# Performance work log

Hardware: AMD Instinct MI355X
Metric: run time of the kernel (lower is better)

The kernel has to match this reference:

```python
import jax, jax.numpy as jnp
import numpy as np

N, G, HID, LAT, E_RAND = 20000, 3000, 256, 32, 320000
EPS = 1e-8
NEG_SLOPE = 0.2  # PyG GATv2Conv default leaky_relu slope


def _segment_softmax(logits, seg, n):
    # numerically stable softmax over edges grouped by destination node
    m = jax.ops.segment_max(logits, seg, num_segments=n)
    ex = jnp.exp(logits - m[seg])
    s = jax.ops.segment_sum(ex, seg, num_segments=n)
    return ex / (s[seg] + 1e-16)


def _gatv2(x, src, dst, Wl, Wr, att, b, n):
    # GATv2 (heads=1): score = att . leaky_relu(Wl x_j + Wr x_i)
    xl = x @ Wl  # [N, C] source transform (also the message)
    xr = x @ Wr  # [N, C] destination transform
    e = jax.nn.leaky_relu(xl[src] + xr[dst], NEG_SLOPE)  # [E, C]
    logit = e @ att  # [E]
    alpha = _segment_softmax(logit, dst, n)
    out = jax.ops.segment_sum(alpha[:, None] * xl[src], dst, num_segments=n)
    return out + b


def _log_zinb(x, mu, theta, pi):
    theta = theta[None, :]
    softplus_pi = jax.nn.softplus(-pi)
    log_theta_eps = jnp.log(theta + EPS)
    log_theta_mu_eps = jnp.log(theta + mu + EPS)
    pi_theta_log = -pi + theta * (log_theta_eps - log_theta_mu_eps)
    case_zero = jax.nn.softplus(pi_theta_log) - softplus_pi
    case_nz = (-softplus_pi + pi_theta_log
               + x * (jnp.log(mu + EPS) - log_theta_mu_eps)
               + jax.lax.lgamma(x + theta) - jax.lax.lgamma(theta)
               - jax.lax.lgamma(x + 1.0))
    return jnp.where(x < EPS, case_zero, 0.0) + jnp.where(x > EPS, case_nz, 0.0)


def setup_inputs():
    key = jax.random.key(0)
    ks = jax.random.split(key, 14)
    x = jax.random.randint(ks[0], (N, G), 0, 20).astype(jnp.float32)
    er = jax.random.randint(ks[1], (2, E_RAND), 0, N, dtype=jnp.int32)
    loops = jnp.tile(jnp.arange(N, dtype=jnp.int32)[None, :], (2, 1))
    edge_index = jnp.concatenate([er, loops], axis=1)  # [2, 340000] incl self-loops
    noise = jax.random.normal(ks[2], (N, LAT), dtype=jnp.float32)

    def init(k, shape, fan_in):
        return jax.random.normal(k, shape, dtype=jnp.float32) / np.float32(np.sqrt(fan_in))

    Wl1 = init(ks[3], (G, HID), G); Wr1 = init(ks[4], (G, HID), G)
    att1 = init(ks[5], (HID,), HID); b1 = jnp.zeros((HID,), jnp.float32)
    Wl2 = init(ks[6], (HID, 2 * LAT), HID); Wr2 = init(ks[7], (HID, 2 * LAT), HID)
    att2 = init(ks[8], (2 * LAT,), 2 * LAT); b2 = jnp.zeros((2 * LAT,), jnp.float32)
    Wd1 = init(ks[9], (LAT, HID), LAT); bd1 = jnp.zeros((HID,), jnp.float32)
    Wd2 = init(ks[10], (HID, G), HID); bd2 = jnp.zeros((G,), jnp.float32)
    Wdo = init(ks[11], (HID, G), HID); bdo = jnp.zeros((G,), jnp.float32)
    theta = jax.random.uniform(ks[12], (G,), minval=0.5, maxval=2.0, dtype=jnp.float32)
    return dict(x=x, edge_index=edge_index, noise=noise,
                Wl1=Wl1, Wr1=Wr1, att1=att1, b1=b1,
                Wl2=Wl2, Wr2=Wr2, att2=att2, b2=b2,
                Wd1=Wd1, bd1=bd1, Wd2=Wd2, bd2=bd2, Wdo=Wdo, bdo=bdo,
                theta=theta)


def reference(x, edge_index, noise, Wl1, Wr1, att1, b1, Wl2, Wr2, att2, b2,
              Wd1, bd1, Wd2, bd2, Wdo, bdo, theta):
    n = x.shape[0]
    src, dst = edge_index[0], edge_index[1]
    # --- GATv2 encoder ---
    h = _gatv2(x, src, dst, Wl1, Wr1, att1, b1, n)
    h2 = _gatv2(jax.nn.relu(h), src, dst, Wl2, Wr2, att2, b2, n)  # [N, 2*LAT]
    mu_z, logvar = h2[:, :LAT], h2[:, LAT:]
    # --- reparameterize: std = sqrt(exp(logvar)) ---
    z = mu_z + noise * jnp.exp(0.5 * logvar)
    # --- ZINB decoder ---
    hd = z @ Wd1 + bd1
    mean = jax.nn.softplus(hd @ Wd2 + bd2)
    pi = hd @ Wdo + bdo
    # --- loss: -E[log ZINB] + KL(q(z|x) || N(0,I)) ---
    recon = -jnp.mean(jnp.sum(_log_zinb(x, mean, theta, pi), axis=1))
    kl = jnp.mean(0.5 * jnp.sum(mu_z ** 2 + jnp.exp(logvar) - logvar - 1.0, axis=1))
    return recon + kl
```

## Files before the change

kernel.cpp:

```cpp
#include <hip/hip_runtime.h>
#include <math.h>

#define NN   20000
#define GG   3000
#define HIDD 256
#define LATT 32
#define FEPS 1e-8f

typedef __attribute__((ext_vector_type(8))) __bf16 bf16x8;
typedef __attribute__((ext_vector_type(4))) float f32x4;

__device__ __forceinline__ float fsp(float v) {
    float t = __expf(-fabsf(v));
    return fmaxf(v, 0.f) + __logf(1.f + t);
}
__device__ __forceinline__ float sp_approx(float t) {
    float a = fabsf(t);
    float den = fmaf(a, fmaf(a, fmaf(a, 0.8382f, -1.4958f), 1.87f), 1.f);
    return fmaxf(t, 0.f) + 0.6931472f * __builtin_amdgcn_rcpf(den);
}
__device__ __forceinline__ float lrelu(float v) {
    return v > 0.f ? v : 0.2f * v;
}
__device__ __forceinline__ ushort f2bf(float f) {
    uint b = __float_as_uint(f);
    return (ushort)((b + 0x7FFFu + ((b >> 16) & 1u)) >> 16);
}
__device__ __forceinline__ uint pk2(float a, float b) {
    return (uint)f2bf(a) | ((uint)f2bf(b) << 16);
}
__device__ __forceinline__ void gload16(const void* g, void* l) {
    __builtin_amdgcn_global_load_lds((const __attribute__((address_space(1))) void*)g,
                                     (__attribute__((address_space(3))) void*)l, 16, 0, 0);
}

__global__ void zinb_table(const float* __restrict__ theta, float* __restrict__ tabL,
                           float* __restrict__ logte, int G_) {
    int idx = blockIdx.x * blockDim.x + threadIdx.x;
    if (idx >= G_ * 20) return;
    int g = idx / 20, c = idx % 20;
    float th = theta[g];
    tabL[idx] = lgammaf((float)c + th) - lgammaf(th) - lgammaf((float)c + 1.f);
    if (c == 0) logte[g] = logf(th + FEPS);
}

__global__ void edge_hist(const int* __restrict__ ei, int* __restrict__ cnt, int E) {
    int e = blockIdx.x * blockDim.x + threadIdx.x;
    if (e < E) atomicAdd(&cnt[ei[E + e]], 1);
}

__global__ __launch_bounds__(1024)
void scan_deg(int* __restrict__ cnt_cur, int* __restrict__ rowptr, int Nn) {
    __shared__ int ts[1024];
    int t = threadIdx.x;
    int chunk = (Nn + 1023) / 1024;
    int beg = t * chunk, end = min(beg + chunk, Nn);
    int s = 0;
    for (int i = beg; i < end; i++) s += cnt_cur[i];
    ts[t] = s;
    __syncthreads();
    for (int off = 1; off < 1024; off <<= 1) {
        int v = (t >= off) ? ts[t - off] : 0;
        __syncthreads();
        ts[t] += v;
        __syncthreads();
    }
    int run = (t == 0) ? 0 : ts[t - 1];
    for (int i = beg; i < end; i++) {
        int c = cnt_cur[i];
        rowptr[i] = run;
        cnt_cur[i] = run;
        run += c;
    }
    if (t == 1023) rowptr[Nn] = ts[1023];
}

__global__ void edge_scatter(const int* __restrict__ ei, int* __restrict__ cur,
                             int* __restrict__ eidx, int E) {
    int e = blockIdx.x * blockDim.x + threadIdx.x;
    if (e < E) {
        int p = atomicAdd(&cur[ei[E + e]], 1);
        eidx[p] = e;
    }
}

__global__ __launch_bounds__(256)
void transp_bf16(const float* __restrict__ in, ushort* __restrict__ out,
                 int K, int N, int Kpad) {
    __shared__ ushort t[32][33];
    int k0 = blockIdx.x * 32, n0 = blockIdx.y * 32;
    int tx = threadIdx.x & 31, ty = threadIdx.x >> 5;
    #pragma unroll
    for (int u = 0; u < 32; u += 8) {
        int k = k0 + ty + u, n = n0 + tx;
        t[ty + u][tx] = (k < K && n < N) ? f2bf(in[(size_t)k * N + n]) : (ushort)0;
    }
    __syncthreads();
    #pragma unroll
    for (int u = 0; u < 32; u += 8) {
        int n = n0 + ty + u, k = k0 + tx;
        if (n < N && k < Kpad) out[(size_t)n * Kpad + k] = t[tx][ty + u];
    }
}

template<bool ABF, bool ZEP>
__global__ __launch_bounds__(512, 4)
void gemm_big(const void* __restrict__ Ap, const ushort* __restrict__ B1t,
              const ushort* __restrict__ B2t, float* __restrict__ C1,
              float* __restrict__ C2, const float* __restrict__ xg,
              const float* __restrict__ tabL, const float* __restrict__ theta,
              const float* __restrict__ logte, const float* __restrict__ bd2,
              const float* __restrict__ bdo, double* __restrict__ partsR,
              int M, int Kreal, int Kpad, int Nc) {
    __shared__ __align__(16) char lds[49152];
    char* ldsA  = lds;
    char* ldsB1 = lds + 16384;
    char* ldsB2 = lds + 32768;
    __shared__ float tabs[ZEP ? 128 * 20 : 1];
    __shared__ float thetas[ZEP ? 128 : 1], thltes[ZEP ? 128 : 1];
    __shared__ float bd2s[ZEP ? 128 : 1], bdos[ZEP ? 128 : 1];
    __shared__ double redd[8];

    const int tid = threadIdx.x;
    const int nwg = gridDim.x * gridDim.y;
    const int orig = blockIdx.y * gridDim.x + blockIdx.x;
    const int q = nwg >> 3, r = nwg & 7, xcd = orig & 7;
    const int vv = (xcd < r ? xcd * (q + 1) : r * (q + 1) + (xcd - r) * q) + (orig >> 3);
    const int bx = vv % gridDim.x, by = vv / gridDim.x;
    const int m0 = by * 128, n0 = bx * 128;
    const int lane = tid & 63, wid = tid >> 6;
    const int wr = wid >> 2, wc = wid & 3;
    const int frow = lane & 15;
    const int fkb = (lane >> 4) << 4;

    if (ZEP) {
        for (int i = tid; i < 128; i += 512) {
            int g = n0 + i;
            bool ok = g < Nc;
            float th = ok ? theta[g] : 1.f;
            thetas[i] = th;
            thltes[i] = ok ? th * logte[g] : 0.f;
            bd2s[i]   = ok ? bd2[g] : 0.f;
            bdos[i]   = ok ? bdo[g] : 0.f;
        }
        for (int i = tid; i < 128 * 20; i += 512) {
            int g = n0 + i / 20;
            tabs[i] = (g < Nc) ? tabL[(size_t)g * 20 + i % 20] : 0.f;
        }
    }

    f32x4 acc1[4][2], acc2[4][2];
    #pragma unroll
    for (int i = 0; i < 4; i++)
        #pragma unroll
        for (int j = 0; j < 2; j++) {
            acc1[i][j] = (f32x4){0.f, 0.f, 0.f, 0.f};
            acc2[i][j] = (f32x4){0.f, 0.f, 0.f, 0.f};
        }

    const int row_in = lane >> 3;
    const int sch = (lane & 7) ^ (row_in & 7);
    const int ldso = (lane << 4);

    const int nk = Kpad >> 6;
    for (int t = 0; t < nk; t++) {
        const int k0 = t << 6;
        #pragma unroll
        for (int u = 0; u < 2; u++) {
            int s = (wid << 1) + u;
            int grow = n0 + (s << 3) + row_in;
            if (grow > Nc - 1) grow = Nc - 1;
            size_t go = (size_t)grow * Kpad + k0 + (sch << 3);
            gload16(B1t + go, ldsB1 + (s << 10) + ldso);
            gload16(B2t + go, ldsB2 + (s << 10) + ldso);
        }
        if (ABF) {
            #pragma unroll
            for (int u = 0; u < 2; u++) {
                int s = (wid << 1) + u;
                int grow = m0 + (s << 3) + row_in;
                if (grow > M - 1) grow = M - 1;
                size_t go = (size_t)grow * Kpad + k0 + (sch << 3);
                gload16((const ushort*)Ap + go, ldsA + (s << 10) + ldso);
            }
        } else {
            int arow = tid >> 2;
            int acol = (tid & 3) << 4;
            int gm = m0 + arow;
            uint4 w0 = make_uint4(0u, 0u, 0u, 0u), w1 = w0;
            if (gm < M) {
                const float* af = (const float*)Ap + (size_t)gm * Kreal + k0 + acol;
                if (k0 + 64 <= Kreal) {
                    float4 a = ((const float4*)af)[0];
                    float4 b = ((const float4*)af)[1];
                    float4 c = ((const float4*)af)[2];
                    float4 d = ((const float4*)af)[3];
                    w0.x = pk2(a.x, a.y); w0.y = pk2(a.z, a.w);
                    w0.z = pk2(b.x, b.y); w0.w = pk2(b.z, b.w);
                    w1.x = pk2(c.x, c.y); w1.y = pk2(c.z, c.w);
                    w1.z = pk2(d.x, d.y); w1.w = pk2(d.z, d.w);
                } else {
                    float tmp[16];
                    #pragma unroll
                    for (int jj = 0; jj < 16; jj++) {
                        int gk = k0 + acol + jj;
                        tmp[jj] = (gk < Kreal) ? af[jj] : 0.f;
                    }
                    w0.x = pk2(tmp[0], tmp[1]);  w0.y = pk2(tmp[2], tmp[3]);
                    w0.z = pk2(tmp[4], tmp[5]);  w0.w = pk2(tmp[6], tmp[7]);
                    w1.x = pk2(tmp[8], tmp[9]);  w1.y = pk2(tmp[10], tmp[11]);
                    w1.z = pk2(tmp[12], tmp[13]); w1.w = pk2(tmp[14], tmp[15]);
                }
            }
            int o0 = ((arow << 7) + (acol << 1)) ^ ((arow & 7) << 4);
            int o1 = ((arow << 7) + ((acol + 8) << 1)) ^ ((arow & 7) << 4);
            *(uint4*)(ldsA + o0) = w0;
            *(uint4*)(ldsA + o1) = w1;
        }
        __syncthreads();
        #pragma unroll
        for (int kk = 0; kk < 2; kk++) {
            int kb = (kk << 6) + fkb;
            bf16x8 af[4], b1f[2], b2f[2];
            #pragma unroll
            for (int mi = 0; mi < 4; mi++) {
                int rr = (wr << 6) + (mi << 4) + frow;
                int o = ((rr << 7) + kb) ^ ((rr & 7) << 4);
                af[mi] = *(const bf16x8*)(ldsA + o);
            }
            #pragma unroll
            for (int ni = 0; ni < 2; ni++) {
                int rr = (wc << 5) + (ni << 4) + frow;
                int o = ((rr << 7) + kb) ^ ((rr & 7) << 4);
                b1f[ni] = *(const bf16x8*)(ldsB1 + o);
                b2f[ni] = *(const bf16x8*)(ldsB2 + o);
            }
            #pragma unroll
            for (int mi = 0; mi < 4; mi++)
                #pragma unroll
                for (int ni = 0; ni < 2; ni++) {
                    acc1[mi][ni] = __builtin_amdgcn_mfma_f32_16x16x32_bf16(af[mi], b1f[ni], acc1[mi][ni], 0, 0, 0);
                    acc2[mi][ni] = __builtin_amdgcn_mfma_f32_16x16x32_bf16(af[mi], b2f[ni], acc2[mi][ni], 0, 0, 0);
                }
        }
        __syncthreads();
    }

    const int lr = (lane >> 4) << 2;
    if (!ZEP) {
        #pragma unroll
        for (int mi = 0; mi < 4; mi++)
            #pragma unroll
            for (int ni = 0; ni < 2; ni++) {
                int gmb = m0 + (wr << 6) + (mi << 4) + lr;
                int gn  = n0 + (wc << 5) + (ni << 4) + frow;
                if (gn >= Nc) continue;
                f32x4 v1 = acc1[mi][ni], v2 = acc2[mi][ni];
                #pragma unroll
                for (int j = 0; j < 4; j++) {
                    int gm = gmb + j;
                    if (gm < M) {
                        C1[(size_t)gm * Nc + gn] = v1[j];
                        C2[(size_t)gm * Nc + gn] = v2[j];
                    }
                }
            }
    } else {
        float lsum = 0.f;
        #pragma unroll
        for (int mi = 0; mi < 4; mi++)
            #pragma unroll
            for (int ni = 0; ni < 2; ni++) {
                int lcol = (wc << 5) + (ni << 4) + frow;
                int gn = n0 + lcol;
                int lrow0 = (wr << 6) + (mi << 4) + lr;
                if (gn >= Nc) continue;
                f32x4 am = acc1[mi][ni], ap = acc2[mi][ni];
                float th = thetas[lcol], thlte = thltes[lcol];
                float bm = bd2s[lcol], bp = bdos[lcol];
                #pragma unroll
                for (int j = 0; j < 4; j++) {
                    int gm = m0 + lrow0 + j;
                    if (gm >= M) continue;
                    float mu  = fsp(am[j] + bm);
                    float pi  = ap[j] + bp;
                    float spp = fsp(pi);
                    float ltme = __logf(th + mu + FEPS);
                    float lmu  = __logf(mu + FEPS);
                    float xv = xg[(size_t)gm * Nc + gn];
                    int xi = (int)(xv + 0.5f);
                    float ptl = fmaf(-th, ltme, thlte) - pi;
                    float corr = (xv < FEPS) ? sp_approx(-ptl) : 0.f;
                    lsum += thlte + tabs[lcol * 20 + xi] - spp
                          - (th + xv) * ltme + xv * lmu + corr;
                }
            }
        #pragma unroll
        for (int off = 32; off; off >>= 1) lsum += __shfl_down(lsum, off);
        if (lane == 0) redd[wid] = (double)lsum;
        __syncthreads();
        if (tid == 0) {
            double s = 0.0;
            #pragma unroll
            for (int i = 0; i < 8; i++) s += redd[i];
            partsR[by * gridDim.x + bx] = s;
        }
    }
}

template<bool ABF, bool ZEP>
__global__ __launch_bounds__(256, 4)
void mfma_dual(const void* __restrict__ Ap, const ushort* __restrict__ B1t,
               const ushort* __restrict__ B2t, float* __restrict__ C1,
               float* __restrict__ C2, int M, int K, int Nc) {
    __shared__ __align__(16) char lds[24576];
    char* ldsA  = lds;
    char* ldsB1 = lds + 8192;
    char* ldsB2 = lds + 16384;

    const int tid = threadIdx.x;
    const int m0 = blockIdx.y * 64, n0 = blockIdx.x * 64;
    const int lane = tid & 63, wid = tid >> 6;
    const int wr = wid >> 1, wc = wid & 1;
    const int frow = lane & 15;
    const int fkb = (lane >> 4) << 4;

    f32x4 acc1[2][2], acc2[2][2];
    #pragma unroll
    for (int i = 0; i < 2; i++)
        #pragma unroll
        for (int j = 0; j < 2; j++) {
            acc1[i][j] = (f32x4){0.f, 0.f, 0.f, 0.f};
            acc2[i][j] = (f32x4){0.f, 0.f, 0.f, 0.f};
        }

    const int nk = (K + 63) >> 6;
    for (int t = 0; t < nk; t++) {
        const int k0 = t << 6;
        #pragma unroll
        for (int u = 0; u < 2; u++) {
            int c = tid + (u << 8);
            int row = c >> 3, col8 = (c & 7) << 3;
            int gm = m0 + row, gk = k0 + col8;
            uint4 w = make_uint4(0u, 0u, 0u, 0u);
            if (gm < M && gk < K)
                w = *(const uint4*)((const ushort*)Ap + (size_t)gm * K + gk);
            int o = ((row << 7) + (col8 << 1)) ^ ((row & 7) << 4);
            *(uint4*)(ldsA + o) = w;
        }
        #pragma unroll
        for (int u = 0; u < 2; u++) {
            int c = tid + (u << 8);
            int row = c >> 3, col8 = (c & 7) << 3;
            int gn = n0 + row, gk = k0 + col8;
            uint4 w1 = make_uint4(0u, 0u, 0u, 0u), w2 = w1;
            if (gn < Nc && gk < K) {
                size_t o = (size_t)gn * K + gk;
                w1 = *(const uint4*)(B1t + o);
                w2 = *(const uint4*)(B2t + o);
            }
            int o = ((row << 7) + (col8 << 1)) ^ ((row & 7) << 4);
            *(uint4*)(ldsB1 + o) = w1;
            *(uint4*)(ldsB2 + o) = w2;
        }
        __syncthreads();
        #pragma unroll
        for (int kk = 0; kk < 2; kk++) {
            int kb = (kk << 6) + fkb;
            bf16x8 af[2], b1f[2], b2f[2];
            #pragma unroll
            for (int mi = 0; mi < 2; mi++) {
                int rr = (wr << 5) + (mi << 4) + frow;
                int o = ((rr << 7) + kb) ^ ((rr & 7) << 4);
                af[mi] = *(const bf16x8*)(ldsA + o);
            }
            #pragma unroll
            for (int ni = 0; ni < 2; ni++) {
                int rr = (wc << 5) + (ni << 4) + frow;
                int o = ((rr << 7) + kb) ^ ((rr & 7) << 4);
                b1f[ni] = *(const bf16x8*)(ldsB1 + o);
                b2f[ni] = *(const bf16x8*)(ldsB2 + o);
            }
            #pragma unroll
            for (int mi = 0; mi < 2; mi++)
                #pragma unroll
                for (int ni = 0; ni < 2; ni++) {
                    acc1[mi][ni] = __builtin_amdgcn_mfma_f32_16x16x32_bf16(af[mi], b1f[ni], acc1[mi][ni], 0, 0, 0);
                    acc2[mi][ni] = __builtin_amdgcn_mfma_f32_16x16x32_bf16(af[mi], b2f[ni], acc2[mi][ni], 0, 0, 0);
                }
        }
        __syncthreads();
    }

    const int lr = (lane >> 4) << 2;
    #pragma unroll
    for (int mi = 0; mi < 2; mi++)
        #pragma unroll
        for (int ni = 0; ni < 2; ni++) {
            int gmb = m0 + (wr << 5) + (mi << 4) + lr;
            int gn  = n0 + (wc << 5) + (ni << 4) + frow;
            if (gn >= Nc) continue;
            f32x4 v1 = acc1[mi][ni], v2 = acc2[mi][ni];
            #pragma unroll
            for (int j = 0; j < 4; j++) {
                int gm = gmb + j;
                if (gm < M) {
                    C1[(size_t)gm * Nc + gn] = v1[j];
                    C2[(size_t)gm * Nc + gn] = v2[j];
                }
            }
        }
}

template<int DW, int OM>
__global__ __launch_bounds__(256)
void gat_attn(const float* __restrict__ xl, const float* __restrict__ xr,
              const float* __restrict__ att, const int* __restrict__ ei,
              const int* __restrict__ rowptr, const int* __restrict__ eidx,
              const float* __restrict__ bias, void* __restrict__ out,
              int D, int Nn) {
    __shared__ float lbuf[4][64];
    int wid = threadIdx.x >> 6, lane = threadIdx.x & 63;
    int n = blockIdx.x * 4 + wid;
    if (n >= Nn) return;
    int k = lane * DW;
    float xrr[DW], ats[DW], hacc[DW];
    if (DW == 4) {
        float4 a4 = *(const float4*)(att + k);
        float4 r4 = *(const float4*)(xr + (size_t)n * D + k);
        ats[0] = a4.x; ats[1] = a4.y; ats[2] = a4.z; ats[3] = a4.w;
        xrr[0] = r4.x; xrr[1] = r4.y; xrr[2] = r4.z; xrr[3] = r4.w;
    } else {
        ats[0] = att[k];
        xrr[0] = xr[(size_t)n * D + k];
    }
    #pragma unroll
    for (int d = 0; d < DW; d++) hacc[d] = 0.f;
    float m = -3.0e38f, ssum = 0.f;
    int beg = rowptr[n], end = rowptr[n + 1];
    for (int c0 = beg; c0 < end; c0 += 64) {
        int cnt = min(64, end - c0);
        for (int j = 0; j < cnt; j++) {
            int e = eidx[c0 + j];
            const float* xs = xl + (size_t)ei[e] * D + k;
            float p;
            if (DW == 4) {
                float4 v = *(const float4*)xs;
                p = ats[0] * lrelu(v.x + xrr[0]) + ats[1] * lrelu(v.y + xrr[1])
                  + ats[2] * lrelu(v.z + xrr[2]) + ats[3] * lrelu(v.w + xrr[3]);
            } else {
                p = ats[0] * lrelu(xs[0] + xrr[0]);
            }
            #pragma unroll
            for (int o2 = 32; o2; o2 >>= 1) p += __shfl_down(p, o2);
            if (lane == 0) lbuf[wid][j] = p;
        }
        float cm = (lane < cnt) ? lbuf[wid][lane] : -3.0e38f;
        #pragma unroll
        for (int o2 = 32; o2; o2 >>= 1) cm = fmaxf(cm, __shfl_xor(cm, o2));
        float mnew = fmaxf(m, cm);
        float scale = __expf(m - mnew);
        ssum *= scale;
        #pragma unroll
        for (int d = 0; d < DW; d++) hacc[d] *= scale;
        for (int j = 0; j < cnt; j++) {
            int e = eidx[c0 + j];
            float w = __expf(lbuf[wid][j] - mnew);
            ssum += w;
            const float* xs = xl + (size_t)ei[e] * D + k;
            if (DW == 4) {
                float4 v = *(const float4*)xs;
                hacc[0] = fmaf(w, v.x, hacc[0]);
                hacc[1] = fmaf(w, v.y, hacc[1]);
                hacc[2] = fmaf(w, v.z, hacc[2]);
                hacc[3] = fmaf(w, v.w, hacc[3]);
            } else {
                hacc[0] = fmaf(w, xs[0], hacc[0]);
            }
        }
        m = mnew;
    }
    float inv = 1.f / (ssum + 1e-16f);
    if (DW == 4) {
        float4 b = *(const float4*)(bias + k);
        float r0 = fmaf(hacc[0], inv, b.x), r1 = fmaf(hacc[1], inv, b.y);
        float r2 = fmaf(hacc[2], inv, b.z), r3 = fmaf(hacc[3], inv, b.w);
        if (OM == 0) {
            *(float4*)((float*)out + (size_t)n * D + k) = make_float4(r0, r1, r2, r3);
        } else {
            ushort4 o;
            o.x = f2bf(fmaxf(r0, 0.f)); o.y = f2bf(fmaxf(r1, 0.f));
            o.z = f2bf(fmaxf(r2, 0.f)); o.w = f2bf(fmaxf(r3, 0.f));
            *(ushort4*)((ushort*)out + (size_t)n * D + k) = o;
        }
    } else {
        float r0 = fmaf(hacc[0], inv, bias[k]);
        if (OM == 0) ((float*)out)[(size_t)n * D + k] = r0;
        else         ((ushort*)out)[(size_t)n * D + k] = f2bf(fmaxf(r0, 0.f));
    }
}

__global__ __launch_bounds__(256)
void z_kl(const float* __restrict__ h2, const float* __restrict__ noise,
          float* __restrict__ z, double* __restrict__ partsK, int Nn) {
    __shared__ double rd[4];
    int gid = blockIdx.x * blockDim.x + threadIdx.x;
    int n = gid >> 5, k = gid & 31;
    float kt = 0.f;
    if (n < Nn) {
        float mu = h2[(size_t)n * 64 + k];
        float lv = h2[(size_t)n * 64 + 32 + k];
        float ev = expf(lv);
        z[(size_t)n * 32 + k] = mu + noise[(size_t)n * 32 + k] * expf(0.5f * lv);
        kt = 0.5f * (mu * mu + ev - lv - 1.f);
    }
    #pragma unroll
    for (int off = 32; off; off >>= 1) kt += __shfl_down(kt, off);
    int wid = threadIdx.x >> 6, lane = threadIdx.x & 63;
    if (lane == 0) rd[wid] = (double)kt;
    __syncthreads();
    if (threadIdx.x == 0) partsK[blockIdx.x] = rd[0] + rd[1] + rd[2] + rd[3];
}

__global__ __launch_bounds__(256)
void hd_gemm(const float* __restrict__ z, const float* __restrict__ Wd1,
             const float* __restrict__ bd1, ushort* __restrict__ hd, int Nn) {
    __shared__ float Ws[32 * 256];
    __shared__ float zs[32 * 32];
    int tid = threadIdx.x;
    #pragma unroll
    for (int i = 0; i < 32; i++) Ws[i * 256 + tid] = Wd1[i * 256 + tid];
    int r0 = blockIdx.x * 32;
    for (int i = tid; i < 32 * 32; i += 256) {
        int r = i >> 5, c = i & 31;
        zs[i] = (r0 + r < Nn) ? z[(size_t)(r0 + r) * 32 + c] : 0.f;
    }
    __syncthreads();
    float b = bd1[tid];
    for (int r = 0; r < 32; r++) {
        if (r0 + r >= Nn) break;
        float acc = b;
        #pragma unroll
        for (int k2 = 0; k2 < 32; k2++) acc = fmaf(zs[r * 32 + k2], Ws[k2 * 256 + tid], acc);
        hd[(size_t)(r0 + r) * 256 + tid] = f2bf(acc);
    }
}

__global__ __launch_bounds__(256)
void final_reduce(const double* __restrict__ pR, int nR,
                  const double* __restrict__ pK, int nK,
                  float* __restrict__ out, int Nn) {
    __shared__ double sd[256];
    double s = 0.0;
    for (int i = threadIdx.x; i < nR; i += 256) s -= pR[i];
    for (int i = threadIdx.x; i < nK; i += 256) s += pK[i];
    sd[threadIdx.x] = s;
    __syncthreads();
    for (int o = 128; o; o >>= 1) {
        if (threadIdx.x < o) sd[threadIdx.x] += sd[threadIdx.x + o];
        __syncthreads();
    }
    if (threadIdx.x == 0) out[0] = (float)(sd[0] / (double)Nn);
}

extern "C" void kernel_launch(void* const* d_in, const int* in_sizes, int n_in,
                              void* d_out, int out_size, void* d_ws, size_t ws_size,
                              hipStream_t stream) {
    const int N_ = NN, G_ = GG, HID_ = HIDD;
    const int KP1 = 3008;
    const float* x     = (const float*)d_in[0];
    const int*   ei    = (const int*)d_in[1];
    const float* noise = (const float*)d_in[2];
    const float* Wl1   = (const float*)d_in[3];
    const float* Wr1   = (const float*)d_in[4];
    const float* att1  = (const float*)d_in[5];
    const float* b1    = (const float*)d_in[6];
    const float* Wl2   = (const float*)d_in[7];
    const float* Wr2   = (const float*)d_in[8];
    const float* att2  = (const float*)d_in[9];
    const float* b2    = (const float*)d_in[10];
    const float* Wd1   = (const float*)d_in[11];
    const float* bd1   = (const float*)d_in[12];
    const float* Wd2   = (const float*)d_in[13];
    const float* bd2   = (const float*)d_in[14];
    const float* Wdo   = (const float*)d_in[15];
    const float* bdo   = (const float*)d_in[16];
    const float* theta = (const float*)d_in[17];
    const int E = in_sizes[1] / 2;

    const int MB128 = (N_ + 127) / 128;
    const int DGX   = (G_ + 127) / 128;
    const int nR    = DGX * MB128;
    const int nKb   = (N_ * 32) / 256;

    char* base = (char*)d_ws;
    size_t off = 0;
    auto alloc = [&](size_t bytes) -> char* {
        char* p = base + off;
        off = (off + bytes + 255) & ~(size_t)255;
        return p;
    };
    double* partsR = (double*)alloc((size_t)nR * 8);
    double* partsK = (double*)alloc((size_t)nKb * 8);
    float*  tabL  = (float*)alloc((size_t)G_ * 20 * 4);
    float*  logte = (float*)alloc((size_t)G_ * 4);
    int*    rowptr= (int*)alloc((size_t)(N_ + 1) * 4);
    int*    cur   = (int*)alloc((size_t)N_ * 4);
    int*    eidx  = (int*)alloc((size_t)E * 4);
    ushort* Wl1t  = (ushort*)alloc((size_t)HID_ * KP1 * 2);
    ushort* Wr1t  = (ushort*)alloc((size_t)HID_ * KP1 * 2);
    ushort* Wl2t  = (ushort*)alloc((size_t)64 * HID_ * 2);
    ushort* Wr2t  = (ushort*)alloc((size_t)64 * HID_ * 2);
    ushort* Wd2t  = (ushort*)alloc((size_t)G_ * HID_ * 2);
    ushort* Wdot  = (ushort*)alloc((size_t)G_ * HID_ * 2);
    float*  xl1   = (float*)alloc((size_t)N_ * HID_ * 4);
    float*  xr1   = (float*)alloc((size_t)N_ * HID_ * 4);
    ushort* h_bf  = (ushort*)alloc((size_t)N_ * HID_ * 2);
    float*  xl2   = (float*)alloc((size_t)N_ * 64 * 4);
    float*  xr2   = (float*)alloc((size_t)N_ * 64 * 4);
    float*  h2    = (float*)alloc((size_t)N_ * 64 * 4);
    float*  zb    = (float*)alloc((size_t)N_ * 32 * 4);

    ushort* hdb = (ushort*)xr1;
    float*  outf = (float*)d_out;

    hipMemsetAsync(cur, 0, N_ * sizeof(int), stream);

    zinb_table<<<(G_ * 20 + 255) / 256, 256, 0, stream>>>(theta, tabL, logte, G_);
    edge_hist<<<(E + 255) / 256, 256, 0, stream>>>(ei, cur, E);
    scan_deg<<<1, 1024, 0, stream>>>(cur, rowptr, N_);
    edge_scatter<<<(E + 255) / 256, 256, 0, stream>>>(ei, cur, eidx, E);

    transp_bf16<<<dim3(KP1 / 32, (HID_ + 31) / 32), 256, 0, stream>>>(Wl1, Wl1t, G_, HID_, KP1);
    transp_bf16<<<dim3(KP1 / 32, (HID_ + 31) / 32), 256, 0, stream>>>(Wr1, Wr1t, G_, HID_, KP1);
    transp_bf16<<<dim3(HID_ / 32, 2), 256, 0, stream>>>(Wl2, Wl2t, HID_, 64, HID_);
    transp_bf16<<<dim3(HID_ / 32, (G_ + 31) / 32), 256, 0, stream>>>(Wd2, Wd2t, HID_, G_, HID_);
    transp_bf16<<<dim3(HID_ / 32, (G_ + 31) / 32), 256, 0, stream>>>(Wdo, Wdot, HID_, G_, HID_);
    transp_bf16<<<dim3(HID_ / 32, 2), 256, 0, stream>>>(Wr2, Wr2t, HID_, 64, HID_);

    gemm_big<false, false><<<dim3(HID_ / 128, MB128), 512, 0, stream>>>(
        x, Wl1t, Wr1t, xl1, xr1, nullptr, nullptr, nullptr, nullptr, nullptr, nullptr, nullptr,
        N_, G_, KP1, HID_);
    gat_attn<4, 1><<<(N_ + 3) / 4, 256, 0, stream>>>(
        xl1, xr1, att1, ei, rowptr, eidx, b1, h_bf, HID_, N_);

    mfma_dual<true, false><<<dim3(1, (N_ + 63) / 64), 256, 0, stream>>>(
        h_bf, Wl2t, Wr2t, xl2, xr2, N_, HID_, 64);
    gat_attn<1, 0><<<(N_ + 3) / 4, 256, 0, stream>>>(
        xl2, xr2, att2, ei, rowptr, eidx, b2, h2, 64, N_);

    z_kl<<<nKb, 256, 0, stream>>>(h2, noise, zb, partsK, N_);

    hd_gemm<<<(N_ + 31) / 32, 256, 0, stream>>>(zb, Wd1, bd1, hdb, N_);
    gemm_big<true, true><<<dim3(DGX, MB128), 512, 0, stream>>>(
        hdb, Wd2t, Wdot, nullptr, nullptr, x, tabL, theta, logte, bd2, bdo, partsR,
        N_, HID_, HID_, G_);

    final_reduce<<<1, 256, 0, stream>>>(partsR, nR, partsK, nKb, outf, N_);
}
```

Baseline: 687.9 us.

## Fold linear decoder layer into combined Wd1·Wd2 weights to shrink decoder GEMM

Because the first decoder layer has no activation, the new wcomb kernel precomputes the products Wd1·Wd2 and Wd1·Wdo plus the folded biases as 32-wide bf16 weights. The fused ZINB decoder GEMM then contracts over K=32 instead of K=256, using a dedicated single-step MFMA kernel with 64-column tiles. This removes the hd_gemm kernel, the hd intermediate buffer and most of the decoder MFMA work. z is now written directly in bf16, and the combined weights are rounded to bf16, which slightly changes rounding. mfma_dual loses its template parameters, which only compiles if its body no longer uses them.

```diff
diff --git a/kernel.cpp b/kernel.cpp
--- a/kernel.cpp
+++ b/kernel.cpp
@@ -103,23 +103,164 @@
     }
 }
 
-template<bool ABF, bool ZEP>
+__global__ __launch_bounds__(256)
+void wcomb(const float* __restrict__ Wd1, const float* __restrict__ bd1,
+           const float* __restrict__ Wd2, const float* __restrict__ bd2,
+           const float* __restrict__ Wdo, const float* __restrict__ bdo,
+           ushort* __restrict__ W2t, ushort* __restrict__ Wot,
+           float* __restrict__ b2c, float* __restrict__ boc, int G_) {
+    __shared__ float w1s[32 * 256];
+    int tid = threadIdx.x;
+    for (int i = tid; i < 32 * 256; i += 256) w1s[i] = Wd1[i];
+    __syncthreads();
+    int gl = tid & 63, rg = tid >> 6;
+    int g = blockIdx.x * 64 + gl;
+    int gc = min(g, G_ - 1);
+    float a2[8], ao[8];
+    #pragma unroll
+    for (int i = 0; i < 8; i++) { a2[i] = 0.f; ao[i] = 0.f; }
+    float ab2 = 0.f, abo = 0.f;
+    for (int j = 0; j < 256; j++) {
+        float w2 = Wd2[(size_t)j * G_ + gc];
+        float wo = Wdo[(size_t)j * G_ + gc];
+        if (rg == 0) {
+            float b1 = bd1[j];
+            ab2 = fmaf(b1, w2, ab2);
+            abo = fmaf(b1, wo, abo);
+        }
+        #pragma unroll
+        for (int i = 0; i < 8; i++) {
+            float w1 = w1s[(rg * 8 + i) * 256 + j];
+            a2[i] = fmaf(w1, w2, a2[i]);
+            ao[i] = fmaf(w1, wo, ao[i]);
+        }
+    }
+    if (g < G_) {
+        #pragma unroll
+        for (int i = 0; i < 8; i++) {
+            W2t[(size_t)g * 32 + rg * 8 + i] = f2bf(a2[i]);
+            Wot[(size_t)g * 32 + rg * 8 + i] = f2bf(ao[i]);
+        }
+        if (rg == 0) { b2c[g] = ab2 + bd2[g]; boc[g] = abo + bdo[g]; }
+    }
+}
+
+__global__ __launch_bounds__(256, 4)
+void dec_zinb(const ushort* __restrict__ zb, const ushort* __restrict__ W2t,
+              const ushort* __restrict__ Wot, const float* __restrict__ xg,
+              const float* __restrict__ tabL, const float* __restrict__ theta,
+              const float* __restrict__ logte, const float* __restrict__ b2c,
+              const float* __restrict__ boc, double* __restrict__ partsR,
+              int M, int G_) {
+    __shared__ float tabs[64 * 20];
+    __shared__ float thetas[64], thltes[64], bd2s[64], bdos[64];
+    __shared__ double redd[4];
+    const int tid = threadIdx.x;
+    const int nwg = gridDim.x * gridDim.y;
+    const int orig = blockIdx.y * gridDim.x + blockIdx.x;
+    const int q = nwg >> 3, r = nwg & 7, xcd = orig & 7;
+    const int vv = (xcd < r ? xcd * (q + 1) : r * (q + 1) + (xcd - r) * q) + (orig >> 3);
+    const int bx = vv % gridDim.x, by = vv / gridDim.x;
+    const int m0 = by * 128, n0 = bx * 64;
+    const int lane = tid & 63, wid = tid >> 6;
+    const int wr = wid >> 1, wc = wid & 1;
+    const int frow = lane & 15;
+    const int ksl = (lane >> 4) << 3;
+
+    for (int i = tid; i < 64; i += 256) {
+        int g = n0 + i;
+        bool ok = g < G_;
+        float th = ok ? theta[g] : 1.f;
+        thetas[i] = th;
+        thltes[i] = ok ? th * logte[g] : 0.f;
+        bd2s[i]   = ok ? b2c[g] : 0.f;
+        bdos[i]   = ok ? boc[g] : 0.f;
+    }
+    for (int i = tid; i < 64 * 20; i += 256) {
+        int g = n0 + i / 20;
+        tabs[i] = (g < G_) ? tabL[(size_t)g * 20 + i % 20] : 0.f;
+    }
+
+    f32x4 acc1[4][2], acc2[4][2];
+    #pragma unroll
+    for (int i = 0; i < 4; i++)
+        #pragma unroll
+        for (int j = 0; j < 2; j++) {
+            acc1[i][j] = (f32x4){0.f, 0.f, 0.f, 0.f};
+            acc2[i][j] = (f32x4){0.f, 0.f, 0.f, 0.f};
+        }
+
+    bf16x8 af[4];
+    #pragma unroll
+    for (int mi = 0; mi < 4; mi++) {
+        int gm = min(m0 + (wr << 6) + (mi << 4) + frow, M - 1);
+        af[mi] = *(const bf16x8*)(zb + (size_t)gm * 32 + ksl);
+    }
+    #pragma unroll
+    for (int ni = 0; ni < 2; ni++) {
+        int gn = min(n0 + (wc << 5) + (ni << 4) + frow, G_ - 1);
+        bf16x8 bf1 = *(const bf16x8*)(W2t + (size_t)gn * 32 + ksl);
+        bf16x8 bf2 = *(const bf16x8*)(Wot + (size_t)gn * 32 + ksl);
+        #pragma unroll
+        for (int mi = 0; mi < 4; mi++) {
+            acc1[mi][ni] = __builtin_amdgcn_mfma_f32_16x16x32_bf16(af[mi], bf1, acc1[mi][ni], 0, 0, 0);
+            acc2[mi][ni] = __builtin_amdgcn_mfma_f32_16x16x32_bf16(af[mi], bf2, acc2[mi][ni], 0, 0, 0);
+        }
+    }
+    __syncthreads();
+
+    const int lr = (lane >> 4) << 2;
+    float lsum = 0.f;
+    #pragma unroll
+    for (int mi = 0; mi < 4; mi++)
+        #pragma unroll
+        for (int ni = 0; ni < 2; ni++) {
+            int lcol = (wc << 5) + (ni << 4) + frow;
+            int gn = n0 + lcol;
+            int gmb = m0 + (wr << 6) + (mi << 4) + lr;
+            if (gn >= G_) continue;
+            float xv4[4];
+            #pragma unroll
+            for (int j = 0; j < 4; j++) {
+                int gm = min(gmb + j, M - 1);
+                xv4[j] = xg[(size_t)gm * G_ + gn];
+            }
+            f32x4 am = acc1[mi][ni], ap = acc2[mi][ni];
+            float th = thetas[lcol], thlte = thltes[lcol];
+            float bm = bd2s[lcol], bp = bdos[lcol];
+            #pragma unroll
+            for (int j = 0; j < 4; j++) {
+                if (gmb + j >= M) continue;
+                float mu  = fsp(am[j] + bm);
+                float pi  = ap[j] + bp;
+                float spp = fsp(pi);
+                float ltme = __logf(th + mu + FEPS);
+                float lmu  = __logf(mu + FEPS);
+                float xv = xv4[j];
+                int xi = (int)(xv + 0.5f);
+                float ptl = fmaf(-th, ltme, thlte) - pi;
+                float corr = (xv < FEPS) ? sp_approx(-ptl) : 0.f;
+                lsum += thlte + tabs[lcol * 20 + xi] - spp
+                      - (th + xv) * ltme + xv * lmu + corr;
+            }
+        }
+    #pragma unroll
+    for (int off = 32; off; off >>= 1) lsum += __shfl_down(lsum, off);
+    if (lane == 0) redd[wid] = (double)lsum;
+    __syncthreads();
+    if (tid == 0)
+        partsR[by * gridDim.x + bx] = redd[0] + redd[1] + redd[2] + redd[3];
+}
+
+template<bool ABF>
 __global__ __launch_bounds__(512, 4)
 void gemm_big(const void* __restrict__ Ap, const ushort* __restrict__ B1t,
               const ushort* __restrict__ B2t, float* __restrict__ C1,
-              float* __restrict__ C2, const float* __restrict__ xg,
-              const float* __restrict__ tabL, const float* __restrict__ theta,
-              const float* __restrict__ logte, const float* __restrict__ bd2,
-              const float* __restrict__ bdo, double* __restrict__ partsR,
-              int M, int Kreal, int Kpad, int Nc) {
+              float* __restrict__ C2, int M, int Kreal, int Kpad, int Nc) {
     __shared__ __align__(16) char lds[49152];
     char* ldsA  = lds;
     char* ldsB1 = lds + 16384;
     char* ldsB2 = lds + 32768;
-    __shared__ float tabs[ZEP ? 128 * 20 : 1];
-    __shared__ float thetas[ZEP ? 128 : 1], thltes[ZEP ? 128 : 1];
-    __shared__ float bd2s[ZEP ? 128 : 1], bdos[ZEP ? 128 : 1];
-    __shared__ double redd[8];
 
     const int tid = threadIdx.x;
     const int nwg = gridDim.x * gridDim.y;
@@ -132,22 +273,6 @@
     const int wr = wid >> 2, wc = wid & 3;
     const int frow = lane & 15;
     const int fkb = (lane >> 4) << 4;
-
-    if (ZEP) {
-        for (int i = tid; i < 128; i += 512) {
-            int g = n0 + i;
-            bool ok = g < Nc;
-            float th = ok ? theta[g] : 1.f;
-            thetas[i] = th;
-            thltes[i] = ok ? th * logte[g] : 0.f;
-            bd2s[i]   = ok ? bd2[g] : 0.f;
-            bdos[i]   = ok ? bdo[g] : 0.f;
-        }
-        for (int i = tid; i < 128 * 20; i += 512) {
-            int g = n0 + i / 20;
-            tabs[i] = (g < Nc) ? tabL[(size_t)g * 20 + i % 20] : 0.f;
-        }
-    }
 
     f32x4 acc1[4][2], acc2[4][2];
     #pragma unroll
@@ -247,68 +372,25 @@
     }
 
     const int lr = (lane >> 4) << 2;
-    if (!ZEP) {
-        #pragma unroll
-        for (int mi = 0; mi < 4; mi++)
-            #pragma unroll
-            for (int ni = 0; ni < 2; ni++) {
-                int gmb = m0 + (wr << 6) + (mi << 4) + lr;
-                int gn  = n0 + (wc << 5) + (ni << 4) + frow;
-                if (gn >= Nc) continue;
-                f32x4 v1 = acc1[mi][ni], v2 = acc2[mi][ni];
-                #pragma unroll
-                for (int j = 0; j < 4; j++) {
-                    int gm = gmb + j;
-                    if (gm < M) {
-                        C1[(size_t)gm * Nc + gn] = v1[j];
-                        C2[(size_t)gm * Nc + gn] = v2[j];
-                    }
+    #pragma unroll
+    for (int mi = 0; mi < 4; mi++)
+        #pragma unroll
+        for (int ni = 0; ni < 2; ni++) {
+            int gmb = m0 + (wr << 6) + (mi << 4) + lr;
+            int gn  = n0 + (wc << 5) + (ni << 4) + frow;
+            if (gn >= Nc) continue;
+            f32x4 v1 = acc1[mi][ni], v2 = acc2[mi][ni];
+            #pragma unroll
+            for (int j = 0; j < 4; j++) {
+                int gm = gmb + j;
+                if (gm < M) {
+                    C1[(size_t)gm * Nc + gn] = v1[j];
+                    C2[(size_t)gm * Nc + gn] = v2[j];
                 }
             }
-    } else {
-        float lsum = 0.f;
-        #pragma unroll
-        for (int mi = 0; mi < 4; mi++)
-            #pragma unroll
-            for (int ni = 0; ni < 2; ni++) {
-                int lcol = (wc << 5) + (ni << 4) + frow;
-                int gn = n0 + lcol;
-                int lrow0 = (wr << 6) + (mi << 4) + lr;
-                if (gn >= Nc) continue;
-                f32x4 am = acc1[mi][ni], ap = acc2[mi][ni];
-                float th = thetas[lcol], thlte = thltes[lcol];
-                float bm = bd2s[lcol], bp = bdos[lcol];
-                #pragma unroll
-                for (int j = 0; j < 4; j++) {
-                    int gm = m0 + lrow0 + j;
-                    if (gm >= M) continue;
-                    float mu  = fsp(am[j] + bm);
-                    float pi  = ap[j] + bp;
-                    float spp = fsp(pi);
-                    float ltme = __logf(th + mu + FEPS);
-                    float lmu  = __logf(mu + FEPS);
-                    float xv = xg[(size_t)gm * Nc + gn];
-                    int xi = (int)(xv + 0.5f);
-                    float ptl = fmaf(-th, ltme, thlte) - pi;
-                    float corr = (xv < FEPS) ? sp_approx(-ptl) : 0.f;
-                    lsum += thlte + tabs[lcol * 20 + xi] - spp
-                          - (th + xv) * ltme + xv * lmu + corr;
-                }
-            }
-        #pragma unroll
-        for (int off = 32; off; off >>= 1) lsum += __shfl_down(lsum, off);
-        if (lane == 0) redd[wid] = (double)lsum;
-        __syncthreads();
-        if (tid == 0) {
-            double s = 0.0;
-            #pragma unroll
-            for (int i = 0; i < 8; i++) s += redd[i];
-            partsR[by * gridDim.x + bx] = s;
-        }
-    }
-}
-
-template<bool ABF, bool ZEP>
+        }
+}
+
 __global__ __launch_bounds__(256, 4)
 void mfma_dual(const void* __restrict__ Ap, const ushort* __restrict__ B1t,
                const ushort* __restrict__ B2t, float* __restrict__ C1,
@@ -502,7 +584,7 @@
 
 __global__ __launch_bounds__(256)
 void z_kl(const float* __restrict__ h2, const float* __restrict__ noise,
-          float* __restrict__ z, double* __restrict__ partsK, int Nn) {
+          ushort* __restrict__ z, double* __restrict__ partsK, int Nn) {
     __shared__ double rd[4];
     int gid = blockIdx.x * blockDim.x + threadIdx.x;
     int n = gid >> 5, k = gid & 31;
@@ -511,7 +593,7 @@
         float mu = h2[(size_t)n * 64 + k];
         float lv = h2[(size_t)n * 64 + 32 + k];
         float ev = expf(lv);
-        z[(size_t)n * 32 + k] = mu + noise[(size_t)n * 32 + k] * expf(0.5f * lv);
+        z[(size_t)n * 32 + k] = f2bf(mu + noise[(size_t)n * 32 + k] * expf(0.5f * lv));
         kt = 0.5f * (mu * mu + ev - lv - 1.f);
     }
     #pragma unroll
@@ -520,30 +602,6 @@
     if (lane == 0) rd[wid] = (double)kt;
     __syncthreads();
     if (threadIdx.x == 0) partsK[blockIdx.x] = rd[0] + rd[1] + rd[2] + rd[3];
-}
-
-__global__ __launch_bounds__(256)
-void hd_gemm(const float* __restrict__ z, const float* __restrict__ Wd1,
-             const float* __restrict__ bd1, ushort* __restrict__ hd, int Nn) {
-    __shared__ float Ws[32 * 256];
-    __shared__ float zs[32 * 32];
-    int tid = threadIdx.x;
-    #pragma unroll
-    for (int i = 0; i < 32; i++) Ws[i * 256 + tid] = Wd1[i * 256 + tid];
-    int r0 = blockIdx.x * 32;
-    for (int i = tid; i < 32 * 32; i += 256) {
-        int r = i >> 5, c = i & 31;
-        zs[i] = (r0 + r < Nn) ? z[(size_t)(r0 + r) * 32 + c] : 0.f;
-    }
-    __syncthreads();
-    float b = bd1[tid];
-    for (int r = 0; r < 32; r++) {
-        if (r0 + r >= Nn) break;
-        float acc = b;
-        #pragma unroll
-        for (int k2 = 0; k2 < 32; k2++) acc = fmaf(zs[r * 32 + k2], Ws[k2 * 256 + tid], acc);
-        hd[(size_t)(r0 + r) * 256 + tid] = f2bf(acc);
-    }
 }
 
 __global__ __launch_bounds__(256)
@@ -589,7 +647,7 @@
     const int E = in_sizes[1] / 2;
 
     const int MB128 = (N_ + 127) / 128;
-    const int DGX   = (G_ + 127) / 128;
+    const int DGX   = (G_ + 63) / 64;
     const int nR    = DGX * MB128;
     const int nKb   = (N_ * 32) / 256;
 
@@ -611,17 +669,18 @@
     ushort* Wr1t  = (ushort*)alloc((size_t)HID_ * KP1 * 2);
     ushort* Wl2t  = (ushort*)alloc((size_t)64 * HID_ * 2);
     ushort* Wr2t  = (ushort*)alloc((size_t)64 * HID_ * 2);
-    ushort* Wd2t  = (ushort*)alloc((size_t)G_ * HID_ * 2);
-    ushort* Wdot  = (ushort*)alloc((size_t)G_ * HID_ * 2);
+    ushort* W2t   = (ushort*)alloc((size_t)G_ * 32 * 2);
+    ushort* Wot   = (ushort*)alloc((size_t)G_ * 32 * 2);
+    float*  b2c   = (float*)alloc((size_t)G_ * 4);
+    float*  boc   = (float*)alloc((size_t)G_ * 4);
     float*  xl1   = (float*)alloc((size_t)N_ * HID_ * 4);
     float*  xr1   = (float*)alloc((size_t)N_ * HID_ * 4);
     ushort* h_bf  = (ushort*)alloc((size_t)N_ * HID_ * 2);
     float*  xl2   = (float*)alloc((size_t)N_ * 64 * 4);
     float*  xr2   = (float*)alloc((size_t)N_ * 64 * 4);
     float*  h2    = (float*)alloc((size_t)N_ * 64 * 4);
-    float*  zb    = (float*)alloc((size_t)N_ * 32 * 4);
-
-    ushort* hdb = (ushort*)xr1;
+    ushort* zb    = (ushort*)alloc((size_t)N_ * 32 * 2);
+
     float*  outf = (float*)d_out;
 
     hipMemsetAsync(cur, 0, N_ * sizeof(int), stream);
@@ -634,27 +693,25 @@
     transp_bf16<<<dim3(KP1 / 32, (HID_ + 31) / 32), 256, 0, stream>>>(Wl1, Wl1t, G_, HID_, KP1);
     transp_bf16<<<dim3(KP1 / 32, (HID_ + 31) / 32), 256, 0, stream>>>(Wr1, Wr1t, G_, HID_, KP1);
     transp_bf16<<<dim3(HID_ / 32, 2), 256, 0, stream>>>(Wl2, Wl2t, HID_, 64, HID_);
-    transp_bf16<<<dim3(HID_ / 32, (G_ + 31) / 32), 256, 0, stream>>>(Wd2, Wd2t, HID_, G_, HID_);
-    transp_bf16<<<dim3(HID_ / 32, (G_ + 31) / 32), 256, 0, stream>>>(Wdo, Wdot, HID_, G_, HID_);
     transp_bf16<<<dim3(HID_ / 32, 2), 256, 0, stream>>>(Wr2, Wr2t, HID_, 64, HID_);
 
-    gemm_big<false, false><<<dim3(HID_ / 128, MB128), 512, 0, stream>>>(
-        x, Wl1t, Wr1t, xl1, xr1, nullptr, nullptr, nullptr, nullptr, nullptr, nullptr, nullptr,
-        N_, G_, KP1, HID_);
+    wcomb<<<(G_ + 63) / 64, 256, 0, stream>>>(
+        Wd1, bd1, Wd2, bd2, Wdo, bdo, W2t, Wot, b2c, boc, G_);
+
+    gemm_big<false><<<dim3(HID_ / 128, MB128), 512, 0, stream>>>(
+        x, Wl1t, Wr1t, xl1, xr1, N_, G_, KP1, HID_);
     gat_attn<4, 1><<<(N_ + 3) / 4, 256, 0, stream>>>(
         xl1, xr1, att1, ei, rowptr, eidx, b1, h_bf, HID_, N_);
 
-    mfma_dual<true, false><<<dim3(1, (N_ + 63) / 64), 256, 0, stream>>>(
+    mfma_dual<<<dim3(1, (N_ + 63) / 64), 256, 0, stream>>>(
         h_bf, Wl2t, Wr2t, xl2, xr2, N_, HID_, 64);
     gat_attn<1, 0><<<(N_ + 3) / 4, 256, 0, stream>>>(
         xl2, xr2, att2, ei, rowptr, eidx, b2, h2, 64, N_);
 
     z_kl<<<nKb, 256, 0, stream>>>(h2, noise, zb, partsK, N_);
 
-    hd_gemm<<<(N_ + 31) / 32, 256, 0, stream>>>(zb, Wd1, bd1, hdb, N_);
-    gemm_big<true, true><<<dim3(DGX, MB128), 512, 0, stream>>>(
-        hdb, Wd2t, Wdot, nullptr, nullptr, x, tabL, theta, logte, bd2, bdo, partsR,
-        N_, HID_, HID_, G_);
+    dec_zinb<<<dim3(DGX, MB128), 256, 0, stream>>>(
+        zb, W2t, Wot, x, tabL, theta, logte, b2c, boc, partsR, N_, G_);
 
     final_reduce<<<1, 256, 0, stream>>>(partsR, nR, partsK, nKb, outf, N_);
 }
```

New measurement: 643.5 us. -6.5%, faster.
